# Performance work log

Measured on AMD Instinct MI355X. Metric: run time of the kernel, lower is better.

Reference implementation:

```python
import jax, jax.numpy as jnp
import numpy as np

B, NP, NJ, ND = 16, 64, 15, 128
SIGMA = 15.0        # cfg.MULTI_PERSON.POSE_SIGMA
BIG = 1.0e5         # sentinel used to mask padded reference persons
EPS = 1e-8


def setup_inputs() -> dict:
    key = jax.random.key(0)
    k1, k2, k3, k4, k5 = jax.random.split(key, 5)
    # 3D plane-sweep hypotheses in the reference camera frame (z>0 so projection is safe)
    uv = jax.random.uniform(k1, (B, NP, NJ, ND, 2), minval=-0.5, maxval=0.5)
    z = jax.random.uniform(k2, (B, NP, NJ, ND, 1), minval=2.0, maxval=10.0)
    poses_3d = jnp.concatenate([uv * z, z], axis=-1).astype(jnp.float32)
    # detected 2D poses in the reference view, pixel coordinates
    poses_2d_ref = (jax.random.uniform(k3, (B, NP, NJ, 2)) * jnp.array([1920.0, 1080.0], jnp.float32)).astype(jnp.float32)
    vis_ref = (jax.random.uniform(k4, (B, NP, NJ)) < 0.8).astype(jnp.float32)
    num_persons_ref = jax.random.randint(k5, (B,), 1, NP + 1).astype(jnp.int32)
    R = jnp.tile(jnp.eye(3, dtype=jnp.float32), (B, 1, 1))
    T = jnp.zeros((B, 3), jnp.float32)
    f = jnp.full((B, 2), 1000.0, jnp.float32)
    c = jnp.tile(jnp.array([960.0, 540.0], jnp.float32), (B, 1))
    image_w = jnp.full((B,), 1920.0, jnp.float32)
    image_h = jnp.full((B,), 1080.0, jnp.float32)
    return dict(poses_3d=poses_3d, poses_2d_ref=poses_2d_ref, vis_ref=vis_ref,
                num_persons_ref=num_persons_ref, R=R, T=T, f=f, c=c,
                image_w=image_w, image_h=image_h)


def _project(pts, R, T, f, c):
    # pinhole projection: x_cam = R (X - T); 2d = f * xy/z + c
    xc = jnp.einsum('bij,bpkdj->bpkdi', R, pts - T[:, None, None, None, :])
    z = xc[..., 2:3]
    return f[:, None, None, None, :] * xc[..., :2] / z + c[:, None, None, None, :]


def reference(poses_3d, poses_2d_ref, vis_ref, num_persons_ref, R, T, f, c, image_w, image_h):
    # 1) project 3D hypotheses to the reference view -> [B,NP,NJ,ND,2]
    p2t = _project(poses_3d, R, T, f, c)
    # 2) visibility-weighted mean pairwise squared distance, expanded as
    #    |a|^2 + |b|^2 - 2 a.b to avoid the [B,NP,NP,NJ,ND,2] intermediate
    pt2 = jnp.sum(p2t ** 2, axis=-1)                      # [B,NP,NJ,ND]
    pr2 = jnp.sum(poses_2d_ref ** 2, axis=-1)             # [B,NQ,NJ]
    wpr = poses_2d_ref * vis_ref[..., None]               # [B,NQ,NJ,2]
    term1 = jnp.einsum('bpjd,bqj->bpqd', pt2, vis_ref)
    term2 = jnp.sum(pr2 * vis_ref, axis=-1)               # [B,NQ]
    term3 = jnp.einsum('bpjdc,bqjc->bpqd', p2t, wpr)
    vsum = jnp.sum(vis_ref, axis=-1)                      # [B,NQ]
    dist = (term1 + term2[:, None, :, None] - 2.0 * term3) / (vsum[:, None, :, None] + EPS)
    # 3) mask padded reference persons, nearest-pose matching
    valid = jnp.arange(NP)[None, :] < num_persons_ref[:, None]   # [B,NQ]
    dist = jnp.where(valid[:, None, :, None], dist, BIG)
    mm = jnp.argmin(dist, axis=2)                          # [B,NP,ND]
    # 4) gather matched 2D poses / visibilities
    b_idx = jnp.arange(B)[:, None, None]
    matched = jnp.transpose(poses_2d_ref[b_idx, mm], (0, 1, 3, 2, 4))  # [B,NP,NJ,ND,2]
    mvis = jnp.transpose(vis_ref[b_idx, mm], (0, 1, 3, 2))             # [B,NP,NJ,ND]
    # 5) exp score (non-panoptic branch) and in-image bounding
    mdist = jnp.sum((p2t - matched) ** 2, axis=-1)
    score = jnp.exp(-mdist / (SIGMA ** 2))
    iw = image_w[:, None, None, None]
    ih = image_h[:, None, None, None]
    inb = ((p2t[..., 0] >= 0) & (p2t[..., 1] >= 0) &
           (p2t[..., 0] <= iw - 1) & (p2t[..., 1] <= ih - 1)).astype(score.dtype)
    bounding = inb * mvis
    return score * bounding
```

## Files before the change

kernel.cpp:

```cpp
#include <hip/hip_runtime.h>

#define NPERS 64
#define NJOINT 15
#define NDEPTH 128
#define BIGF 100000.0f
#define EPSF 1e-8f
#define INFF 3.0e38f

__global__ __launch_bounds__(256, 4)
void pose_match_kernel(
    const float* __restrict__ poses_3d,
    const float* __restrict__ p2d,
    const float* __restrict__ vis,
    const int*   __restrict__ nper,
    const float* __restrict__ Rm,
    const float* __restrict__ Tm,
    const float* __restrict__ fm,
    const float* __restrict__ cm,
    const float* __restrict__ iw_,
    const float* __restrict__ ih_,
    float* __restrict__ out)
{
    const int b    = blockIdx.x >> 6;
    const int rem  = blockIdx.x & 63;
    const int pp   = rem >> 1;
    const int dh   = rem & 1;
    const int p0   = pp * 2;
    const int tid  = threadIdx.x;
    const int lane = tid & 63;
    const int d    = dh * 64 + lane;
    const int wvs  = __builtin_amdgcn_readfirstlane(tid >> 6);

    __shared__ float4 sq[NPERS][NJOINT];
    __shared__ float4 sco2[NJOINT][48];
    __shared__ float  sc_c[NPERS];
    __shared__ float  bvred[4][2][64];
    __shared__ int    bqred[4][2][64];

    for (int i = tid; i < NPERS * NJOINT; i += 256) {
        int q = i / NJOINT, j = i % NJOINT;
        float v  = vis[(b * NPERS + q) * NJOINT + j];
        float rx = p2d[((b * NPERS + q) * NJOINT + j) * 2 + 0];
        float ry = p2d[((b * NPERS + q) * NJOINT + j) * 2 + 1];
        sq[q][j] = make_float4(v, rx, ry, 0.0f);
    }
    __syncthreads();

    if (wvs == 3) {
        const int q = lane;
        float vs = 0.0f, t2 = 0.0f;
        #pragma unroll
        for (int j = 0; j < NJOINT; ++j) {
            float4 s = sq[q][j];
            vs += s.x;
            t2 = fmaf(s.y * s.y + s.z * s.z, s.x, t2);
        }
        float inv = 1.0f / (vs + EPSF);
        #pragma unroll
        for (int j = 0; j < NJOINT; ++j) {
            float4 s = sq[q][j];
            float* row = (float*)&sco2[j][0];
            row[q * 3 + 0] = s.x * inv;
            row[q * 3 + 1] = 2.0f * s.x * s.y * inv;
            row[q * 3 + 2] = 2.0f * s.x * s.z * inv;
        }
        sc_c[q] = t2 * inv;
    }
    __syncthreads();

    const float R00 = Rm[b*9+0], R01 = Rm[b*9+1], R02 = Rm[b*9+2];
    const float R10 = Rm[b*9+3], R11 = Rm[b*9+4], R12 = Rm[b*9+5];
    const float R20 = Rm[b*9+6], R21 = Rm[b*9+7], R22 = Rm[b*9+8];
    const float T0 = Tm[b*3+0], T1 = Tm[b*3+1], T2 = Tm[b*3+2];
    const float fx = fm[b*2+0], fy = fm[b*2+1];
    const float cx = cm[b*2+0], cy = cm[b*2+1];
    const float iwm1 = iw_[b] - 1.0f;
    const float ihm1 = ih_[b] - 1.0f;
    const int   npv  = nper[b];

    const int q0  = wvs * 16;
    const int nvs = __builtin_amdgcn_readfirstlane(
                        min(max(npv - q0, 0), 16));

    const float* pA = poses_3d +
        ((size_t)(b * NPERS + p0    ) * NJOINT * NDEPTH + d) * 3;
    const float* pB = poses_3d +
        ((size_t)(b * NPERS + p0 + 1) * NJOINT * NDEPTH + d) * 3;

    float acc0[16], acc1[16];
    #pragma unroll
    for (int k = 0; k < 16; ++k) { acc0[k] = 0.0f; acc1[k] = 0.0f; }

#define JSTEP(J, GCOUNT)                                                      \
    {                                                                         \
        const int off = (J) * NDEPTH * 3;                                     \
        float X0, Y0, X1, Y1;                                                 \
        {                                                                     \
            float a0 = pA[off + 0] - T0;                                      \
            float a1 = pA[off + 1] - T1;                                      \
            float a2 = pA[off + 2] - T2;                                      \
            float xc0 = R00 * a0 + R01 * a1 + R02 * a2;                       \
            float xc1 = R10 * a0 + R11 * a1 + R12 * a2;                       \
            float xc2 = R20 * a0 + R21 * a1 + R22 * a2;                       \
            float r   = __builtin_amdgcn_rcpf(xc2);                           \
            X0 = fmaf(fx * xc0, r, cx);                                       \
            Y0 = fmaf(fy * xc1, r, cy);                                       \
        }                                                                     \
        {                                                                     \
            float a0 = pB[off + 0] - T0;                                      \
            float a1 = pB[off + 1] - T1;                                      \
            float a2 = pB[off + 2] - T2;                                      \
            float xc0 = R00 * a0 + R01 * a1 + R02 * a2;                       \
            float xc1 = R10 * a0 + R11 * a1 + R12 * a2;                       \
            float xc2 = R20 * a0 + R21 * a1 + R22 * a2;                       \
            float r   = __builtin_amdgcn_rcpf(xc2);                           \
            X1 = fmaf(fx * xc0, r, cx);                                       \
            Y1 = fmaf(fy * xc1, r, cy);                                       \
        }                                                                     \
        _Pragma("unroll")                                                     \
        for (int g = 0; g < (GCOUNT); ++g) {                                  \
            float4 r0 = sco2[J][wvs * 12 + g * 3 + 0];                        \
            float4 r1 = sco2[J][wvs * 12 + g * 3 + 1];                        \
            float4 r2 = sco2[J][wvs * 12 + g * 3 + 2];                        \
            ACC1(0, r0.x, r0.y, r0.z)                                         \
            ACC1(1, r0.w, r1.x, r1.y)                                         \
            ACC1(2, r1.z, r1.w, r2.x)                                         \
            ACC1(3, r2.y, r2.z, r2.w)                                         \
        }                                                                     \
    }

#define ACC1(K, W, WX, WY)                                                    \
    {                                                                         \
        float u;                                                              \
        u = fmaf((W), X0, -(WX));                                             \
        acc0[g * 4 + K] = fmaf(X0, u, acc0[g * 4 + K]);                       \
        u = fmaf((W), Y0, -(WY));                                             \
        acc0[g * 4 + K] = fmaf(Y0, u, acc0[g * 4 + K]);                       \
        u = fmaf((W), X1, -(WX));                                             \
        acc1[g * 4 + K] = fmaf(X1, u, acc1[g * 4 + K]);                       \
        u = fmaf((W), Y1, -(WY));                                             \
        acc1[g * 4 + K] = fmaf(Y1, u, acc1[g * 4 + K]);                       \
    }

    if (nvs == 16) {
        #pragma unroll 2
        for (int j = 0; j < NJOINT; ++j) {
            JSTEP(j, 4)
        }
    } else if (nvs > 0) {
        #pragma unroll 1
        for (int j = 0; j < NJOINT; ++j) {
            const int ng = (nvs + 3) >> 2;
            if (ng == 4)      { JSTEP(j, 4) }
            else if (ng == 3) { JSTEP(j, 3) }
            else if (ng == 2) { JSTEP(j, 2) }
            else              { JSTEP(j, 1) }
        }
    }
#undef ACC1
#undef JSTEP

    float bv0, bv1;
    int   bq0, bq1;
    if (npv < NPERS) { bv0 = bv1 = BIGF; bq0 = bq1 = npv; }
    else             { bv0 = bv1 = INFF; bq0 = bq1 = 0;   }
    #pragma unroll
    for (int k = 0; k < 16; ++k) {
        if (k < nvs) {
            float cterm = sc_c[q0 + k];
            float d0 = acc0[k] + cterm;
            float d1 = acc1[k] + cterm;
            if (d0 < bv0) { bv0 = d0; bq0 = q0 + k; }
            if (d1 < bv1) { bv1 = d1; bq1 = q0 + k; }
        }
    }
    bvred[wvs][0][lane] = bv0;  bqred[wvs][0][lane] = bq0;
    bvred[wvs][1][lane] = bv1;  bqred[wvs][1][lane] = bq1;
    __syncthreads();

#define EPILOGUE(PI, PAR, PPTR)                                               \
    if (wvs == (PI) * 2 + (PAR)) {                                            \
        float bestv = bvred[0][PI][lane];                                     \
        int   bestq = bqred[0][PI][lane];                                     \
        _Pragma("unroll")                                                     \
        for (int k = 1; k < 4; ++k) {                                         \
            float v  = bvred[k][PI][lane];                                    \
            int   qq = bqred[k][PI][lane];                                    \
            if (v < bestv || (v == bestv && qq < bestq)) {                    \
                bestv = v; bestq = qq;                                        \
            }                                                                 \
        }                                                                     \
        const int obase = ((b * NPERS + p0 + PI) * NJOINT) * NDEPTH + d;      \
        _Pragma("unroll")                                                     \
        for (int j = (PAR); j < NJOINT; j += 2) {                             \
            const int off = j * NDEPTH * 3;                                   \
            float a0 = PPTR[off + 0] - T0;                                    \
            float a1 = PPTR[off + 1] - T1;                                    \
            float a2 = PPTR[off + 2] - T2;                                    \
            float xc0 = R00 * a0 + R01 * a1 + R02 * a2;                       \
            float xc1 = R10 * a0 + R11 * a1 + R12 * a2;                       \
            float xc2 = R20 * a0 + R21 * a1 + R22 * a2;                       \
            float r   = __builtin_amdgcn_rcpf(xc2);                           \
            float xx  = fmaf(fx * xc0, r, cx);                                \
            float yy  = fmaf(fy * xc1, r, cy);                                \
            float4 v = sq[bestq][j];                                          \
            float dx = xx - v.y;                                              \
            float dy = yy - v.z;                                              \
            float md = fmaf(dx, dx, dy * dy);                                 \
            float sc = __expf(-md * (1.0f / 225.0f));                         \
            float inb = (xx >= 0.0f && yy >= 0.0f &&                          \
                         xx <= iwm1 && yy <= ihm1) ? 1.0f : 0.0f;             \
            out[obase + j * NDEPTH] = sc * inb * v.x;                         \
        }                                                                     \
    }

    EPILOGUE(0, 0, pA)
    EPILOGUE(0, 1, pA)
    EPILOGUE(1, 0, pB)
    EPILOGUE(1, 1, pB)
#undef EPILOGUE
}

extern "C" void kernel_launch(void* const* d_in, const int* in_sizes, int n_in,
                              void* d_out, int out_size, void* d_ws, size_t ws_size,
                              hipStream_t stream) {
    const float* poses_3d = (const float*)d_in[0];
    const float* p2d      = (const float*)d_in[1];
    const float* vis      = (const float*)d_in[2];
    const int*   nper     = (const int*)d_in[3];
    const float* Rm       = (const float*)d_in[4];
    const float* Tm       = (const float*)d_in[5];
    const float* fm       = (const float*)d_in[6];
    const float* cm       = (const float*)d_in[7];
    const float* iw       = (const float*)d_in[8];
    const float* ih       = (const float*)d_in[9];
    float* out = (float*)d_out;

    const int B = in_sizes[3];
    dim3 grid(B * 64);
    dim3 block(256);
    pose_match_kernel<<<grid, block, 0, stream>>>(
        poses_3d, p2d, vis, nper, Rm, Tm, fm, cm, iw, ih, out);
}
```

Before: 29.60 us.

## Precompute per-reference coefficients in a separate kernel and read them from global memory

Moves the per-reference-person coefficient computation (normalized visibility weights and constant term) out of every block into a small prelaunch kernel that writes them to the workspace. The main kernel drops one barrier and the single-wave serial coefficient phase, and now reads the coefficients through uniform global/scalar loads instead of LDS. The cost is an extra kernel launch and a dependence on cached global reads inside the hot joint loop. The sq shared fill is kept but appears unused before the epilogue, with no barrier left after it.

```diff
diff --git a/kernel.cpp b/kernel.cpp
--- a/kernel.cpp
+++ b/kernel.cpp
@@ -6,6 +6,37 @@
 #define BIGF 100000.0f
 #define EPSF 1e-8f
 #define INFF 3.0e38f
+
+
+__global__ __launch_bounds__(256) void coef_kernel(
+    const float* __restrict__ p2d,
+    const float* __restrict__ vis,
+    float* __restrict__ ws,
+    int total)
+{
+    int t = blockIdx.x * 256 + threadIdx.x;
+    if (t >= total) return;
+    const int b = t >> 6, q = t & 63;
+    float v[NJOINT], rx[NJOINT], ry[NJOINT];
+    float vs = 0.0f, t2 = 0.0f;
+    #pragma unroll
+    for (int j = 0; j < NJOINT; ++j) {
+        v[j]  = vis[t * NJOINT + j];
+        rx[j] = p2d[(t * NJOINT + j) * 2 + 0];
+        ry[j] = p2d[(t * NJOINT + j) * 2 + 1];
+        vs += v[j];
+        t2 = fmaf(rx[j] * rx[j] + ry[j] * ry[j], v[j], t2);
+    }
+    float inv = 1.0f / (vs + EPSF);
+    float* gco = ws + (size_t)b * NJOINT * 192;
+    #pragma unroll
+    for (int j = 0; j < NJOINT; ++j) {
+        gco[j * 192 + q * 3 + 0] = v[j] * inv;
+        gco[j * 192 + q * 3 + 1] = 2.0f * v[j] * rx[j] * inv;
+        gco[j * 192 + q * 3 + 2] = 2.0f * v[j] * ry[j] * inv;
+    }
+    ws[(size_t)16 * NJOINT * 192 + b * NPERS + q] = t2 * inv;
+}
 
 __global__ __launch_bounds__(256, 4)
 void pose_match_kernel(
@@ -19,6 +50,7 @@
     const float* __restrict__ cm,
     const float* __restrict__ iw_,
     const float* __restrict__ ih_,
+    const float* __restrict__ ws,
     float* __restrict__ out)
 {
     const int b    = blockIdx.x >> 6;
@@ -32,8 +64,6 @@
     const int wvs  = __builtin_amdgcn_readfirstlane(tid >> 6);
 
     __shared__ float4 sq[NPERS][NJOINT];
-    __shared__ float4 sco2[NJOINT][48];
-    __shared__ float  sc_c[NPERS];
     __shared__ float  bvred[4][2][64];
     __shared__ int    bqred[4][2][64];
 
@@ -44,29 +74,6 @@
         float ry = p2d[((b * NPERS + q) * NJOINT + j) * 2 + 1];
         sq[q][j] = make_float4(v, rx, ry, 0.0f);
     }
-    __syncthreads();
-
-    if (wvs == 3) {
-        const int q = lane;
-        float vs = 0.0f, t2 = 0.0f;
-        #pragma unroll
-        for (int j = 0; j < NJOINT; ++j) {
-            float4 s = sq[q][j];
-            vs += s.x;
-            t2 = fmaf(s.y * s.y + s.z * s.z, s.x, t2);
-        }
-        float inv = 1.0f / (vs + EPSF);
-        #pragma unroll
-        for (int j = 0; j < NJOINT; ++j) {
-            float4 s = sq[q][j];
-            float* row = (float*)&sco2[j][0];
-            row[q * 3 + 0] = s.x * inv;
-            row[q * 3 + 1] = 2.0f * s.x * s.y * inv;
-            row[q * 3 + 2] = 2.0f * s.x * s.z * inv;
-        }
-        sc_c[q] = t2 * inv;
-    }
-    __syncthreads();
 
     const float R00 = Rm[b*9+0], R01 = Rm[b*9+1], R02 = Rm[b*9+2];
     const float R10 = Rm[b*9+3], R11 = Rm[b*9+4], R12 = Rm[b*9+5];
@@ -86,6 +93,9 @@
         ((size_t)(b * NPERS + p0    ) * NJOINT * NDEPTH + d) * 3;
     const float* pB = poses_3d +
         ((size_t)(b * NPERS + p0 + 1) * NJOINT * NDEPTH + d) * 3;
+
+    const float* gcb = ws + (size_t)b * NJOINT * 192;
+    const float* gcc = ws + (size_t)16 * NJOINT * 192 + b * NPERS;
 
     float acc0[16], acc1[16];
     #pragma unroll
@@ -117,11 +127,12 @@
             X1 = fmaf(fx * xc0, r, cx);                                       \
             Y1 = fmaf(fy * xc1, r, cy);                                       \
         }                                                                     \
+        const float4* cb4 = (const float4*)(gcb + (J) * 192 + wvs * 48);      \
         _Pragma("unroll")                                                     \
         for (int g = 0; g < (GCOUNT); ++g) {                                  \
-            float4 r0 = sco2[J][wvs * 12 + g * 3 + 0];                        \
-            float4 r1 = sco2[J][wvs * 12 + g * 3 + 1];                        \
-            float4 r2 = sco2[J][wvs * 12 + g * 3 + 2];                        \
+            float4 r0 = cb4[g * 3 + 0];                                       \
+            float4 r1 = cb4[g * 3 + 1];                                       \
+            float4 r2 = cb4[g * 3 + 2];                                       \
             ACC1(0, r0.x, r0.y, r0.z)                                         \
             ACC1(1, r0.w, r1.x, r1.y)                                         \
             ACC1(2, r1.z, r1.w, r2.x)                                         \
@@ -167,7 +178,7 @@
     #pragma unroll
     for (int k = 0; k < 16; ++k) {
         if (k < nvs) {
-            float cterm = sc_c[q0 + k];
+            float cterm = gcc[q0 + k];
             float d0 = acc0[k] + cterm;
             float d1 = acc1[k] + cterm;
             if (d0 < bv0) { bv0 = d0; bq0 = q0 + k; }
@@ -235,10 +246,15 @@
     const float* iw       = (const float*)d_in[8];
     const float* ih       = (const float*)d_in[9];
     float* out = (float*)d_out;
+    float* ws  = (float*)d_ws;
 
     const int B = in_sizes[3];
+    const int total = B * NPERS;
+
+    coef_kernel<<<(total + 255) / 256, 256, 0, stream>>>(p2d, vis, ws, total);
+
     dim3 grid(B * 64);
     dim3 block(256);
     pose_match_kernel<<<grid, block, 0, stream>>>(
-        poses_3d, p2d, vis, nper, Rm, Tm, fm, cm, iw, ih, out);
+        poses_3d, p2d, vis, nper, Rm, Tm, fm, cm, iw, ih, ws, out);
 }
```

Result: slower. 34.72 us (+17.3%).
